# Performance work log

Hardware: AMD Instinct MI355X
Metric: run time of the kernel (lower is better)

Reference implementation:

```python
import jax, jax.numpy as jnp
import numpy as np

EMB, NH, NG, T_MAX = 2048, 16, 4, 2048
HD = EMB // NH          # 128
HPG = NH // NG          # 4
B, T = 2, 2048


def _rope_tables(t):
    inv_freq = 1.0 / (10000.0 ** (jnp.arange(0, HD, 2, dtype=jnp.float32) / HD))
    freqs = jnp.outer(jnp.arange(t, dtype=jnp.float32), inv_freq)  # [t, HD//2]
    return jnp.cos(freqs), jnp.sin(freqs)


def _apply_rope(x, cos, sin):
    # x: [..., t, HD], interleaved pairs (0::2 real, 1::2 imag)
    x1 = x[..., 0::2]
    x2 = x[..., 1::2]
    r1 = x1 * cos - x2 * sin
    r2 = x1 * sin + x2 * cos
    return jnp.stack([r1, r2], axis=-1).reshape(x.shape)


def setup_inputs() -> dict:
    key = jax.random.key(0)
    ks = jax.random.split(key, 5)
    s = 0.02
    return {
        "x": jax.random.normal(ks[0], (B, T, EMB), dtype=jnp.float32),
        "Wq": jax.random.normal(ks[1], (EMB, EMB), dtype=jnp.float32) * s,
        "Wk": jax.random.normal(ks[2], (NG * HD, EMB), dtype=jnp.float32) * s,
        "Wv": jax.random.normal(ks[3], (NG * HD, EMB), dtype=jnp.float32) * s,
        "Wo": jax.random.normal(ks[4], (EMB, EMB), dtype=jnp.float32) * s,
    }


def reference(x, Wq, Wk, Wv, Wo):
    b, t, _ = x.shape
    cos, sin = _rope_tables(t)  # [t, HD//2] each; broadcast over batch/heads

    # projections (torch Linear: x @ W.T)
    q = (x @ Wq.T).reshape(b, t, NH, HD).transpose(0, 2, 1, 3)  # [b, NH, t, HD]
    k = (x @ Wk.T).reshape(b, t, NG, HD).transpose(0, 2, 1, 3)  # [b, NG, t, HD]
    v = (x @ Wv.T).reshape(b, t, NG, HD).transpose(0, 2, 1, 3)  # [b, NG, t, HD]

    q = _apply_rope(q, cos, sin)
    k = _apply_rope(k, cos, sin)

    # grouped attention without materializing expanded K/V
    qg = q.reshape(b, NG, HPG, t, HD)                       # [b, g, h, t, d]
    scale = 1.0 / jnp.sqrt(jnp.asarray(HD, dtype=x.dtype))
    scores = jnp.einsum('bghtd,bgsd->bghts', qg, k) * scale  # [b, g, h, t, s]

    causal = jnp.tril(jnp.ones((t, t), dtype=bool))
    scores = jnp.where(causal, scores, jnp.finfo(scores.dtype).min)
    attn = jax.nn.softmax(scores, axis=-1)

    out = jnp.einsum('bghts,bgsd->bghtd', attn, v)           # [b, g, h, t, d]
    out = out.reshape(b, NH, t, HD).transpose(0, 2, 1, 3).reshape(b, t, EMB)
    return out @ Wo.T
```

## Files before the change

### kernel.cpp

```cpp
#include <hip/hip_runtime.h>
#include <stdint.h>
#include <math.h>

#define EMB 2048
#define NHq 16
#define NGk 4
#define HD 128
#define Bb 2
#define Tt 2048
#define MROWS (Bb*Tt)
#define QKVN 3072
#define NQT 32

typedef __bf16 bf16x8 __attribute__((ext_vector_type(8)));
typedef float f32x4 __attribute__((ext_vector_type(4)));
typedef unsigned int u32x4 __attribute__((ext_vector_type(4)));
typedef unsigned short u16;
typedef unsigned int u32;

__device__ __forceinline__ u16 f2bf(float f) {
    unsigned int u = __float_as_uint(f);
    u += 0x7fff + ((u >> 16) & 1);
    return (u16)(u >> 16);
}
__device__ __forceinline__ float bf2f(u16 u) {
    return __uint_as_float(((u32)u) << 16);
}
__device__ __forceinline__ u32 cvt_pk_bf16(float lo, float hi) {
    u32 r;
    asm("v_cvt_pk_bf16_f32 %0, %1, %2" : "=v"(r) : "v"(lo), "v"(hi));
    return r;
}

#define GLOAD_LDS16(g, l) \
    __builtin_amdgcn_global_load_lds((const __attribute__((address_space(1))) void*)(g), \
                                     (__attribute__((address_space(3))) void*)(l), 16, 0, 0)

__global__ void cast_bf16_kernel(const float* __restrict__ src, u16* __restrict__ dst, int n4) {
    int i = blockIdx.x * blockDim.x + threadIdx.x;
    if (i < n4) {
        float4 v = reinterpret_cast<const float4*>(src)[i];
        ushort4 o;
        o.x = f2bf(v.x); o.y = f2bf(v.y); o.z = f2bf(v.z); o.w = f2bf(v.w);
        reinterpret_cast<ushort4*>(dst)[i] = o;
    }
}

__global__ void wcast_kernel(const float* __restrict__ Wq, const float* __restrict__ Wk,
                             const float* __restrict__ Wv, const float* __restrict__ Wo,
                             u16* __restrict__ dst) {
    int i = blockIdx.x * blockDim.x + threadIdx.x;
    const float* src; int local;
    if (i < 1048576)      { src = Wq; local = i; }
    else if (i < 1310720) { src = Wk; local = i - 1048576; }
    else if (i < 1572864) { src = Wv; local = i - 1310720; }
    else                  { src = Wo; local = i - 1572864; }
    float4 v = reinterpret_cast<const float4*>(src)[local];
    ushort4 o;
    o.x = f2bf(v.x); o.y = f2bf(v.y); o.z = f2bf(v.z); o.w = f2bf(v.w);
    reinterpret_cast<ushort4*>(dst)[i] = o;
}

__global__ void rope_tables_kernel(float* __restrict__ ctab, float* __restrict__ stab) {
    int t = blockIdx.x, i = threadIdx.x;
    float inv = powf(10000.f, -2.f * (float)i / (float)HD);
    float ang = (float)t * inv;
    ctab[t * 64 + i] = cosf(ang);
    stab[t * 64 + i] = sinf(ang);
}

__global__ void rope_qk_kernel(const u16* __restrict__ lin, const float* __restrict__ ctab,
                               const float* __restrict__ stab, u16* __restrict__ Qb,
                               u16* __restrict__ Kb, float qscale) {
    int i = threadIdx.x;
    int tt = blockIdx.x * 4 + threadIdx.y;
    int hh = blockIdx.y, b = blockIdx.z;
    int coloff; u16* out; float scale;
    if (hh < NHq) { coloff = hh * HD; scale = qscale;
                    out = Qb + (((size_t)(b * NHq + hh)) * Tt + tt) * HD; }
    else { int g = hh - NHq; coloff = EMB + g * HD; scale = 1.f;
           out = Kb + (((size_t)(b * NGk + g)) * Tt + tt) * HD; }
    u32 pair = *reinterpret_cast<const u32*>(&lin[((size_t)(b * Tt + tt)) * QKVN + coloff + 2 * i]);
    float x1 = bf2f((u16)(pair & 0xffff)), x2 = bf2f((u16)(pair >> 16));
    float c = ctab[tt * 64 + i], s = stab[tt * 64 + i];
    ushort2 o;
    o.x = f2bf((x1 * c - x2 * s) * scale);
    o.y = f2bf((x1 * s + x2 * c) * scale);
    *reinterpret_cast<ushort2*>(&out[2 * i]) = o;
}

__global__ void vtrans_kernel(const u16* __restrict__ lin, u16* __restrict__ vt) {
    int tx = threadIdx.x, dy = threadIdx.y;
    int tt = blockIdx.x * 64 + tx;
    int g = blockIdx.y, b = blockIdx.z;
    int ttp = (tt & ~31) | (((tt >> 2) & 3) * 8 + ((tt >> 4) & 1) * 4 + (tt & 3));
    const u16* src = &lin[((size_t)(b * Tt + tt)) * QKVN + EMB + NGk * HD + g * HD];
    u16* dst = &vt[(((size_t)(b * NGk + g)) * HD) * Tt + ttp];
    #pragma unroll
    for (int k = 0; k < 16; ++k) {
        int d = dy + k * 8;
        dst[(size_t)d * Tt] = src[d];
    }
}

template<int OUTBF>
__global__ __launch_bounds__(256) void gemm_bt(const u16* __restrict__ A, const u16* __restrict__ W,
                                               void* __restrict__ Cout, int M, int N, int K) {
    __shared__ u16 Atile[128 * 32];
    __shared__ u16 Btile[128 * 32];
    const int brow = blockIdx.x * 128;
    const int bcol = blockIdx.y * 128;
    const int t = threadIdx.x;
    const int w = t >> 6, l = t & 63;
    const int lr = l & 15, lq = l >> 4;
    const int wr = (w >> 1) * 64, wc = (w & 1) * 64;
    f32x4 acc[4][4] = {};
    const int nkt = K >> 5;
    for (int kt = 0; kt < nkt; ++kt) {
        const int k0 = kt * 32;
        #pragma unroll
        for (int i = 0; i < 2; ++i) {
            int f = i * 256 + t;
            int row = f >> 2, cb = (f & 3) * 8;
            GLOAD_LDS16(A + (size_t)(brow + row) * K + k0 + cb, &Atile[(i * 256 + w * 64) * 8]);
            GLOAD_LDS16(W + (size_t)(bcol + row) * K + k0 + cb, &Btile[(i * 256 + w * 64) * 8]);
        }
        __syncthreads();
        bf16x8 a[4], b[4];
        #pragma unroll
        for (int m = 0; m < 4; ++m)
            a[m] = *reinterpret_cast<const bf16x8*>(&Atile[(wr + m * 16 + lr) * 32 + lq * 8]);
        #pragma unroll
        for (int n = 0; n < 4; ++n)
            b[n] = *reinterpret_cast<const bf16x8*>(&Btile[(wc + n * 16 + lr) * 32 + lq * 8]);
        #pragma unroll
        for (int m = 0; m < 4; ++m)
            #pragma unroll
            for (int n = 0; n < 4; ++n)
                acc[m][n] = __builtin_amdgcn_mfma_f32_16x16x32_bf16(a[m], b[n], acc[m][n], 0, 0, 0);
        __syncthreads();
    }
    #pragma unroll
    for (int m = 0; m < 4; ++m)
        #pragma unroll
        for (int n = 0; n < 4; ++n)
            #pragma unroll
            for (int r = 0; r < 4; ++r) {
                size_t idx = (size_t)(brow + wr + m * 16 + lq * 4 + r) * N + bcol + wc + n * 16 + lr;
                if (OUTBF) ((u16*)Cout)[idx] = f2bf(acc[m][n][r]);
                else       ((float*)Cout)[idx] = acc[m][n][r];
            }
}

__global__ __launch_bounds__(512) void flash_attn(const u16* __restrict__ Q, const u16* __restrict__ K,
                                                  const u16* __restrict__ Vt, u16* __restrict__ Out) {
    __shared__ __align__(16) char smem[69632];
    u16* KldsBase = (u16*)smem;
    u16* VldsBase = (u16*)(smem + 32768);
    const int h = blockIdx.y;
    const int b = blockIdx.z;
    const int ilo = (b == 0) ? blockIdx.x : (NQT / 2 - 1 - blockIdx.x);
    const int ihi = NQT - 1 - ilo;
    const int g = h >> 2;
    const int t = threadIdx.x;
    const int w = t >> 6, l = t & 63;
    const int wq = w & 3, half = w >> 2;
    const int lr = l & 15, lq = l >> 4;

    const size_t qhead = ((size_t)(b * NHq + h)) * Tt;
    const size_t qblo = (qhead + ilo * 64 + wq * 16) * HD;
    const size_t qbhi = (qhead + ihi * 64 + wq * 16) * HD;
    bf16x8 qfl[4], qfh[4];
    #pragma unroll
    for (int d = 0; d < 4; ++d) {
        qfl[d] = *reinterpret_cast<const bf16x8*>(&Q[qblo + (size_t)lr * HD + d * 32 + lq * 8]);
        qfh[d] = *reinterpret_cast<const bf16x8*>(&Q[qbhi + (size_t)lr * HD + d * 32 + lq * 8]);
    }
    bf16x8 ones;
    #pragma unroll
    for (int j = 0; j < 8; ++j) ones[j] = (__bf16)1.0f;

    f32x4 ol[8] = {}, oh[8] = {};
    f32x4 lsl = {}, lsh = {};

    const int qlo = ilo * 64 + wq * 16 + lr;
    const int qhi = ihi * 64 + wq * 16 + lr;
    const size_t kbase  = ((size_t)(b * NGk + g)) * Tt * HD;
    const size_t vtbase = ((size_t)(b * NGk + g)) * HD * Tt;
    const int nkt = NQT - ilo;

    int kofs[2], vofs[2];
    #pragma unroll
    for (int j = 0; j < 2; ++j) {
        int krow = j * 32 + w * 4 + (l >> 4);
        kofs[j] = krow * HD + (((l & 15) ^ (krow & 7)) * 8);
        int vrow = j * 64 + w * 8 + (l >> 3);
        vofs[j] = vrow * (int)Tt + (((l & 7) ^ (vrow & 7)) * 8);
    }

    #pragma unroll
    for (int j = 0; j < 2; ++j) {
        GLOAD_LDS16(K + kbase + kofs[j], KldsBase + (j * 512 + w * 64) * 8);
        GLOAD_LDS16(Vt + vtbase + vofs[j], VldsBase + (j * 512 + w * 64) * 8);
    }
    int cur = 0;

    for (int kt = 0; kt < nkt; ++kt) {
        const int kp0 = kt * 64;
        __syncthreads();
        if (kt + 1 < nkt) {
            #pragma unroll
            for (int j = 0; j < 2; ++j) {
                GLOAD_LDS16(K + kbase + (size_t)(kp0 + 64) * HD + kofs[j],
                            KldsBase + (cur ^ 1) * 8192 + (j * 512 + w * 64) * 8);
                GLOAD_LDS16(Vt + vtbase + (kp0 + 64) + vofs[j],
                            VldsBase + (cur ^ 1) * 8192 + (j * 512 + w * 64) * 8);
            }
        }
        const char* Kb = smem + cur * 16384;
        const char* Vb = smem + 32768 + cur * 16384;

        const bool lo_act = (kt <= ilo);
        f32x4 sl[2] = {}, sh[2] = {};
        __builtin_amdgcn_s_setprio(1);
        #pragma unroll
        for (int ct = 0; ct < 2; ++ct) {
            #pragma unroll
            for (int d = 0; d < 4; ++d) {
                int row = half * 32 + ct * 16 + lr;
                int bo = row * 256 + ((d * 64 + lq * 16) ^ ((row & 7) << 4));
                bf16x8 kf = *reinterpret_cast<const bf16x8*>(Kb + bo);
                sh[ct] = __builtin_amdgcn_mfma_f32_16x16x32_bf16(kf, qfh[d], sh[ct], 0, 0, 0);
                if (lo_act) sl[ct] = __builtin_amdgcn_mfma_f32_16x16x32_bf16(kf, qfl[d], sl[ct], 0, 0, 0);
            }
        }
        __builtin_amdgcn_s_setprio(0);

        const int kvb = kp0 + half * 32 + lq * 4;
        bf16x8 pfh, pfl;
        {
            const bool diag = (kt == nkt - 1);
            float e[2][4];
            #pragma unroll
            for (int ct = 0; ct < 2; ++ct)
                #pragma unroll
                for (int r = 0; r < 4; ++r)
                    e[ct][r] = exp2f(sh[ct][r]);
            if (diag) {
                #pragma unroll
                for (int ct = 0; ct < 2; ++ct)
                    #pragma unroll
                    for (int r = 0; r < 4; ++r)
                        if (kvb + ct * 16 + r > qhi) e[ct][r] = 0.f;
            }
            u32x4 pk;
            pk[0] = cvt_pk_bf16(e[0][0], e[0][1]);
            pk[1] = cvt_pk_bf16(e[0][2], e[0][3]);
            pk[2] = cvt_pk_bf16(e[1][0], e[1][1]);
            pk[3] = cvt_pk_bf16(e[1][2], e[1][3]);
            pfh = __builtin_bit_cast(bf16x8, pk);
        }
        if (lo_act) {
            const bool diag = (kt == ilo);
            float e[2][4];
            #pragma unroll
            for (int ct = 0; ct < 2; ++ct)
                #pragma unroll
                for (int r = 0; r < 4; ++r)
                    e[ct][r] = exp2f(sl[ct][r]);
            if (diag) {
                #pragma unroll
                for (int ct = 0; ct < 2; ++ct)
                    #pragma unroll
                    for (int r = 0; r < 4; ++r)
                        if (kvb + ct * 16 + r > qlo) e[ct][r] = 0.f;
            }
            u32x4 pk;
            pk[0] = cvt_pk_bf16(e[0][0], e[0][1]);
            pk[1] = cvt_pk_bf16(e[0][2], e[0][3]);
            pk[2] = cvt_pk_bf16(e[1][0], e[1][1]);
            pk[3] = cvt_pk_bf16(e[1][2], e[1][3]);
            pfl = __builtin_bit_cast(bf16x8, pk);
        }

        __builtin_amdgcn_s_setprio(1);
        #pragma unroll
        for (int n = 0; n < 8; ++n) {
            int vrow = n * 16 + lr;
            int bv = vrow * 128 + ((half * 64 + lq * 16) ^ ((vrow & 7) << 4));
            bf16x8 vf = *reinterpret_cast<const bf16x8*>(Vb + bv);
            oh[n] = __builtin_amdgcn_mfma_f32_16x16x32_bf16(vf, pfh, oh[n], 0, 0, 0);
            if (lo_act) ol[n] = __builtin_amdgcn_mfma_f32_16x16x32_bf16(vf, pfl, ol[n], 0, 0, 0);
        }
        lsh = __builtin_amdgcn_mfma_f32_16x16x32_bf16(ones, pfh, lsh, 0, 0, 0);
        if (lo_act) lsl = __builtin_amdgcn_mfma_f32_16x16x32_bf16(ones, pfl, lsl, 0, 0, 0);
        __builtin_amdgcn_s_setprio(0);
        cur ^= 1;
    }

    __syncthreads();
    float* Osh = (float*)smem;
    float* Lsh = (float*)(smem + 128 * 132 * 4);
    if (half == 1) {
        #pragma unroll
        for (int n = 0; n < 8; ++n) {
            *reinterpret_cast<f32x4*>(&Osh[(wq * 32 + lr) * 132 + n * 16 + lq * 4]) = oh[n];
            *reinterpret_cast<f32x4*>(&Osh[(wq * 32 + 16 + lr) * 132 + n * 16 + lq * 4]) = ol[n];
        }
        if (lq == 0) {
            Lsh[wq * 32 + lr] = lsh[0];
            Lsh[wq * 32 + 16 + lr] = lsl[0];
        }
    }
    __syncthreads();
    if (half == 0) {
        const float invh = 1.f / (lsh[0] + Lsh[wq * 32 + lr]);
        const float invl = 1.f / (lsl[0] + Lsh[wq * 32 + 16 + lr]);
        u16* outh = Out + ((size_t)(b * Tt) + ihi * 64 + wq * 16 + lr) * EMB + h * HD;
        u16* outl = Out + ((size_t)(b * Tt) + ilo * 64 + wq * 16 + lr) * EMB + h * HD;
        #pragma unroll
        for (int n = 0; n < 8; ++n) {
            f32x4 sh4 = *reinterpret_cast<const f32x4*>(&Osh[(wq * 32 + lr) * 132 + n * 16 + lq * 4]);
            f32x4 sl4 = *reinterpret_cast<const f32x4*>(&Osh[(wq * 32 + 16 + lr) * 132 + n * 16 + lq * 4]);
            uint2 ph, pl;
            ph.x = cvt_pk_bf16((oh[n][0] + sh4[0]) * invh, (oh[n][1] + sh4[1]) * invh);
            ph.y = cvt_pk_bf16((oh[n][2] + sh4[2]) * invh, (oh[n][3] + sh4[3]) * invh);
            pl.x = cvt_pk_bf16((ol[n][0] + sl4[0]) * invl, (ol[n][1] + sl4[1]) * invl);
            pl.y = cvt_pk_bf16((ol[n][2] + sl4[2]) * invl, (ol[n][3] + sl4[3]) * invl);
            *reinterpret_cast<uint2*>(&outh[n * 16 + lq * 4]) = ph;
            *reinterpret_cast<uint2*>(&outl[n * 16 + lq * 4]) = pl;
        }
    }
}

extern "C" void kernel_launch(void* const* d_in, const int* in_sizes, int n_in,
                              void* d_out, int out_size, void* d_ws, size_t ws_size,
                              hipStream_t stream) {
    (void)in_sizes; (void)n_in; (void)out_size; (void)ws_size;
    const float* x  = (const float*)d_in[0];
    const float* Wq = (const float*)d_in[1];
    const float* Wk = (const float*)d_in[2];
    const float* Wv = (const float*)d_in[3];
    const float* Wo = (const float*)d_in[4];
    float* out = (float*)d_out;

    char* ws = (char*)d_ws;
    size_t off = 0;
    auto alloc = [&](size_t bytes) { char* p = ws + off; off += (bytes + 255) & ~(size_t)255; return p; };

    u16* w_bf    = (u16*)alloc((size_t)(QKVN * EMB + EMB * EMB) * 2);
    u16* x_bf    = (u16*)alloc((size_t)MROWS * EMB * 2);
    u16* qkv_lin = (u16*)alloc((size_t)MROWS * QKVN * 4);
    u16* Qb      = (u16*)alloc((size_t)Bb * NHq * Tt * HD * 2);
    u16* Kb      = (u16*)alloc((size_t)Bb * NGk * Tt * HD * 2);
    u16* Vtb     = (u16*)alloc((size_t)Bb * NGk * HD * Tt * 2);
    float* ctab  = (float*)alloc((size_t)Tt * 64 * 4);
    float* stab  = (float*)alloc((size_t)Tt * 64 * 4);
    u16* attnout = qkv_lin;

    u16* wo_bf = w_bf + (size_t)QKVN * EMB;

    cast_bf16_kernel<<<(MROWS * EMB / 4 + 255) / 256, 256, 0, stream>>>(x, x_bf, MROWS * EMB / 4);
    wcast_kernel<<<(QKVN * EMB + EMB * EMB) / 4 / 256, 256, 0, stream>>>(Wq, Wk, Wv, Wo, w_bf);
    rope_tables_kernel<<<Tt, 64, 0, stream>>>(ctab, stab);

    gemm_bt<1><<<dim3(MROWS / 128, QKVN / 128), 256, 0, stream>>>(x_bf, w_bf, qkv_lin, MROWS, QKVN, EMB);

    const float qscale = 1.44269504088896f / sqrtf((float)HD);
    rope_qk_kernel<<<dim3(Tt / 4, NHq + NGk, Bb), dim3(64, 4), 0, stream>>>(qkv_lin, ctab, stab, Qb, Kb, qscale);
    vtrans_kernel<<<dim3(Tt / 64, NGk, Bb), dim3(64, 8), 0, stream>>>(qkv_lin, Vtb);

    flash_attn<<<dim3(NQT / 2, NHq, Bb), 512, 0, stream>>>(Qb, Kb, Vtb, attnout);

    gemm_bt<0><<<dim3(MROWS / 128, EMB / 128), 256, 0, stream>>>(attnout, wo_bf, out, MROWS, EMB, EMB);
}
```

Measured before the change: 240.7 us.

## Software-pipeline attention loop: overlap QK/softmax of tile p with PV of tile p-1

Restructures the flash attention main loop so each iteration computes scores and softmax for the current KV tile while doing the PV accumulation for the previous tile. The V buffer becomes triple-buffered to allow this, which raises LDS use to 80KB, and the loop gains one extra epilogue iteration. The aim is to let exp and convert work interleave with MFMA work so fewer matrix-core cycles sit idle. The cost is higher register pressure from carrying the previous probability fragments, plus larger LDS that may reduce occupancy.

```diff
diff --git a/kernel.cpp b/kernel.cpp
--- a/kernel.cpp
+++ b/kernel.cpp
@@ -154,7 +154,7 @@
 
 __global__ __launch_bounds__(512) void flash_attn(const u16* __restrict__ Q, const u16* __restrict__ K,
                                                   const u16* __restrict__ Vt, u16* __restrict__ Out) {
-    __shared__ __align__(16) char smem[69632];
+    __shared__ __align__(16) char smem[81920];
     u16* KldsBase = (u16*)smem;
     u16* VldsBase = (u16*)(smem + 32768);
     const int h = blockIdx.y;
@@ -203,99 +203,107 @@
         GLOAD_LDS16(K + kbase + kofs[j], KldsBase + (j * 512 + w * 64) * 8);
         GLOAD_LDS16(Vt + vtbase + vofs[j], VldsBase + (j * 512 + w * 64) * 8);
     }
-    int cur = 0;
-
-    for (int kt = 0; kt < nkt; ++kt) {
-        const int kp0 = kt * 64;
-        __syncthreads();
-        if (kt + 1 < nkt) {
+    __syncthreads();
+
+    bf16x8 pfh_c, pfl_c;
+
+    for (int p = 0; p <= nkt; ++p) {
+        if (p + 1 < nkt) {
+            const size_t kp1 = (size_t)(p + 1) * 64;
+            u16* kd = KldsBase + ((p + 1) & 1) * 8192;
+            u16* vd = VldsBase + ((p + 1) % 3) * 8192;
             #pragma unroll
             for (int j = 0; j < 2; ++j) {
-                GLOAD_LDS16(K + kbase + (size_t)(kp0 + 64) * HD + kofs[j],
-                            KldsBase + (cur ^ 1) * 8192 + (j * 512 + w * 64) * 8);
-                GLOAD_LDS16(Vt + vtbase + (kp0 + 64) + vofs[j],
-                            VldsBase + (cur ^ 1) * 8192 + (j * 512 + w * 64) * 8);
-            }
-        }
-        const char* Kb = smem + cur * 16384;
-        const char* Vb = smem + 32768 + cur * 16384;
-
-        const bool lo_act = (kt <= ilo);
-        f32x4 sl[2] = {}, sh[2] = {};
-        __builtin_amdgcn_s_setprio(1);
-        #pragma unroll
-        for (int ct = 0; ct < 2; ++ct) {
-            #pragma unroll
-            for (int d = 0; d < 4; ++d) {
-                int row = half * 32 + ct * 16 + lr;
-                int bo = row * 256 + ((d * 64 + lq * 16) ^ ((row & 7) << 4));
-                bf16x8 kf = *reinterpret_cast<const bf16x8*>(Kb + bo);
-                sh[ct] = __builtin_amdgcn_mfma_f32_16x16x32_bf16(kf, qfh[d], sh[ct], 0, 0, 0);
-                if (lo_act) sl[ct] = __builtin_amdgcn_mfma_f32_16x16x32_bf16(kf, qfl[d], sl[ct], 0, 0, 0);
-            }
-        }
-        __builtin_amdgcn_s_setprio(0);
-
-        const int kvb = kp0 + half * 32 + lq * 4;
-        bf16x8 pfh, pfl;
-        {
-            const bool diag = (kt == nkt - 1);
-            float e[2][4];
-            #pragma unroll
-            for (int ct = 0; ct < 2; ++ct)
+                GLOAD_LDS16(K + kbase + kp1 * HD + kofs[j], kd + (j * 512 + w * 64) * 8);
+                GLOAD_LDS16(Vt + vtbase + kp1 + vofs[j], vd + (j * 512 + w * 64) * 8);
+            }
+        }
+
+        const bool lo_p = (p <= ilo);
+        bf16x8 pfh_n, pfl_n;
+        if (p < nkt) {
+            const char* Kb = smem + (p & 1) * 16384;
+            f32x4 sl[2] = {}, sh[2] = {};
+            __builtin_amdgcn_s_setprio(1);
+            #pragma unroll
+            for (int ct = 0; ct < 2; ++ct) {
                 #pragma unroll
-                for (int r = 0; r < 4; ++r)
-                    e[ct][r] = exp2f(sh[ct][r]);
-            if (diag) {
+                for (int d = 0; d < 4; ++d) {
+                    int row = half * 32 + ct * 16 + lr;
+                    int bo = row * 256 + ((d * 64 + lq * 16) ^ ((row & 7) << 4));
+                    bf16x8 kf = *reinterpret_cast<const bf16x8*>(Kb + bo);
+                    sh[ct] = __builtin_amdgcn_mfma_f32_16x16x32_bf16(kf, qfh[d], sh[ct], 0, 0, 0);
+                    if (lo_p) sl[ct] = __builtin_amdgcn_mfma_f32_16x16x32_bf16(kf, qfl[d], sl[ct], 0, 0, 0);
+                }
+            }
+            __builtin_amdgcn_s_setprio(0);
+
+            const int kvb = p * 64 + half * 32 + lq * 4;
+            {
+                const bool diag = (p == nkt - 1);
+                float e[2][4];
                 #pragma unroll
                 for (int ct = 0; ct < 2; ++ct)
                     #pragma unroll
                     for (int r = 0; r < 4; ++r)
-                        if (kvb + ct * 16 + r > qhi) e[ct][r] = 0.f;
-            }
-            u32x4 pk;
-            pk[0] = cvt_pk_bf16(e[0][0], e[0][1]);
-            pk[1] = cvt_pk_bf16(e[0][2], e[0][3]);
-            pk[2] = cvt_pk_bf16(e[1][0], e[1][1]);
-            pk[3] = cvt_pk_bf16(e[1][2], e[1][3]);
-            pfh = __builtin_bit_cast(bf16x8, pk);
-        }
-        if (lo_act) {
-            const bool diag = (kt == ilo);
-            float e[2][4];
-            #pragma unroll
-            for (int ct = 0; ct < 2; ++ct)
-                #pragma unroll
-                for (int r = 0; r < 4; ++r)
-                    e[ct][r] = exp2f(sl[ct][r]);
-            if (diag) {
+                        e[ct][r] = exp2f(sh[ct][r]);
+                if (diag) {
+                    #pragma unroll
+                    for (int ct = 0; ct < 2; ++ct)
+                        #pragma unroll
+                        for (int r = 0; r < 4; ++r)
+                            if (kvb + ct * 16 + r > qhi) e[ct][r] = 0.f;
+                }
+                u32x4 pk;
+                pk[0] = cvt_pk_bf16(e[0][0], e[0][1]);
+                pk[1] = cvt_pk_bf16(e[0][2], e[0][3]);
+                pk[2] = cvt_pk_bf16(e[1][0], e[1][1]);
+                pk[3] = cvt_pk_bf16(e[1][2], e[1][3]);
+                pfh_n = __builtin_bit_cast(bf16x8, pk);
+            }
+            if (lo_p) {
+                const bool diag = (p == ilo);
+                float e[2][4];
                 #pragma unroll
                 for (int ct = 0; ct < 2; ++ct)
                     #pragma unroll
                     for (int r = 0; r < 4; ++r)
-                        if (kvb + ct * 16 + r > qlo) e[ct][r] = 0.f;
-            }
-            u32x4 pk;
-            pk[0] = cvt_pk_bf16(e[0][0], e[0][1]);
-            pk[1] = cvt_pk_bf16(e[0][2], e[0][3]);
-            pk[2] = cvt_pk_bf16(e[1][0], e[1][1]);
-            pk[3] = cvt_pk_bf16(e[1][2], e[1][3]);
-            pfl = __builtin_bit_cast(bf16x8, pk);
-        }
-
-        __builtin_amdgcn_s_setprio(1);
-        #pragma unroll
-        for (int n = 0; n < 8; ++n) {
-            int vrow = n * 16 + lr;
-            int bv = vrow * 128 + ((half * 64 + lq * 16) ^ ((vrow & 7) << 4));
-            bf16x8 vf = *reinterpret_cast<const bf16x8*>(Vb + bv);
-            oh[n] = __builtin_amdgcn_mfma_f32_16x16x32_bf16(vf, pfh, oh[n], 0, 0, 0);
-            if (lo_act) ol[n] = __builtin_amdgcn_mfma_f32_16x16x32_bf16(vf, pfl, ol[n], 0, 0, 0);
-        }
-        lsh = __builtin_amdgcn_mfma_f32_16x16x32_bf16(ones, pfh, lsh, 0, 0, 0);
-        if (lo_act) lsl = __builtin_amdgcn_mfma_f32_16x16x32_bf16(ones, pfl, lsl, 0, 0, 0);
-        __builtin_amdgcn_s_setprio(0);
-        cur ^= 1;
+                        e[ct][r] = exp2f(sl[ct][r]);
+                if (diag) {
+                    #pragma unroll
+                    for (int ct = 0; ct < 2; ++ct)
+                        #pragma unroll
+                        for (int r = 0; r < 4; ++r)
+                            if (kvb + ct * 16 + r > qlo) e[ct][r] = 0.f;
+                }
+                u32x4 pk;
+                pk[0] = cvt_pk_bf16(e[0][0], e[0][1]);
+                pk[1] = cvt_pk_bf16(e[0][2], e[0][3]);
+                pk[2] = cvt_pk_bf16(e[1][0], e[1][1]);
+                pk[3] = cvt_pk_bf16(e[1][2], e[1][3]);
+                pfl_n = __builtin_bit_cast(bf16x8, pk);
+            }
+        }
+
+        if (p >= 1) {
+            const char* Vb = smem + 32768 + ((p - 1) % 3) * 16384;
+            const bool lo_prev = (p - 1 <= ilo);
+            __builtin_amdgcn_s_setprio(1);
+            #pragma unroll
+            for (int n = 0; n < 8; ++n) {
+                int vrow = n * 16 + lr;
+                int bv = vrow * 128 + ((half * 64 + lq * 16) ^ ((vrow & 7) << 4));
+                bf16x8 vf = *reinterpret_cast<const bf16x8*>(Vb + bv);
+                oh[n] = __builtin_amdgcn_mfma_f32_16x16x32_bf16(vf, pfh_c, oh[n], 0, 0, 0);
+                if (lo_prev) ol[n] = __builtin_amdgcn_mfma_f32_16x16x32_bf16(vf, pfl_c, ol[n], 0, 0, 0);
+            }
+            lsh = __builtin_amdgcn_mfma_f32_16x16x32_bf16(ones, pfh_c, lsh, 0, 0, 0);
+            if (lo_prev) lsl = __builtin_amdgcn_mfma_f32_16x16x32_bf16(ones, pfl_c, lsl, 0, 0, 0);
+            __builtin_amdgcn_s_setprio(0);
+        }
+        pfh_c = pfh_n;
+        pfl_c = pfl_n;
+        if (p + 1 < nkt) __syncthreads();
     }
 
     __syncthreads();
```

After: 246.4 us. +2.4%, slower.

## Load K/V fragments directly from global into registers, drop LDS staging

Applied to the files above, without the earlier changes.

Attention now reads K and V^T fragments straight from global memory into registers each tile, instead of double-buffering them through LDS with async global-to-LDS loads and barriers. The block index mapping is reordered so the heads sharing a KV group land in neighbouring blocks, which should improve L2 reuse of K/V. The epilogue reduction is split into two passes so LDS shrinks to about 34KB, allowing higher occupancy. The trade-off is that global-load latency is no longer hidden by prefetching, and each wave issues redundant global reads that it depends on via cache hits.

```diff
diff --git a/kernel.cpp b/kernel.cpp
--- a/kernel.cpp
+++ b/kernel.cpp
@@ -154,14 +154,13 @@
 
 __global__ __launch_bounds__(512) void flash_attn(const u16* __restrict__ Q, const u16* __restrict__ K,
                                                   const u16* __restrict__ Vt, u16* __restrict__ Out) {
-    __shared__ __align__(16) char smem[69632];
-    u16* KldsBase = (u16*)smem;
-    u16* VldsBase = (u16*)(smem + 32768);
-    const int h = blockIdx.y;
-    const int b = blockIdx.z;
-    const int ilo = (b == 0) ? blockIdx.x : (NQT / 2 - 1 - blockIdx.x);
+    __shared__ __align__(16) char smem[34816];
+    const int bx = blockIdx.x, by = blockIdx.y, bz = blockIdx.z;
+    const int g = bx & 3, b = (bx >> 2) & 1;
+    const int hh = (bx >> 3) | (bz << 1);
+    const int h = g * 4 + hh;
+    const int ilo = (hh & 1) ? (15 - by) : by;
     const int ihi = NQT - 1 - ilo;
-    const int g = h >> 2;
     const int t = threadIdx.x;
     const int w = t >> 6, l = t & 63;
     const int wq = w & 3, half = w >> 2;
@@ -185,53 +184,34 @@
 
     const int qlo = ilo * 64 + wq * 16 + lr;
     const int qhi = ihi * 64 + wq * 16 + lr;
-    const size_t kbase  = ((size_t)(b * NGk + g)) * Tt * HD;
-    const size_t vtbase = ((size_t)(b * NGk + g)) * HD * Tt;
+    const u16* Kp = K + ((size_t)(b * NGk + g)) * Tt * HD + (size_t)(half * 32 + lr) * HD + lq * 8;
+    const u16* Vp = Vt + ((size_t)(b * NGk + g)) * HD * Tt + (size_t)lr * Tt + half * 32 + lq * 8;
     const int nkt = NQT - ilo;
-
-    int kofs[2], vofs[2];
-    #pragma unroll
-    for (int j = 0; j < 2; ++j) {
-        int krow = j * 32 + w * 4 + (l >> 4);
-        kofs[j] = krow * HD + (((l & 15) ^ (krow & 7)) * 8);
-        int vrow = j * 64 + w * 8 + (l >> 3);
-        vofs[j] = vrow * (int)Tt + (((l & 7) ^ (vrow & 7)) * 8);
-    }
-
-    #pragma unroll
-    for (int j = 0; j < 2; ++j) {
-        GLOAD_LDS16(K + kbase + kofs[j], KldsBase + (j * 512 + w * 64) * 8);
-        GLOAD_LDS16(Vt + vtbase + vofs[j], VldsBase + (j * 512 + w * 64) * 8);
-    }
-    int cur = 0;
 
     for (int kt = 0; kt < nkt; ++kt) {
         const int kp0 = kt * 64;
-        __syncthreads();
-        if (kt + 1 < nkt) {
-            #pragma unroll
-            for (int j = 0; j < 2; ++j) {
-                GLOAD_LDS16(K + kbase + (size_t)(kp0 + 64) * HD + kofs[j],
-                            KldsBase + (cur ^ 1) * 8192 + (j * 512 + w * 64) * 8);
-                GLOAD_LDS16(Vt + vtbase + (kp0 + 64) + vofs[j],
-                            VldsBase + (cur ^ 1) * 8192 + (j * 512 + w * 64) * 8);
-            }
-        }
-        const char* Kb = smem + cur * 16384;
-        const char* Vb = smem + 32768 + cur * 16384;
-
-        const bool lo_act = (kt <= ilo);
+        const bool lo_p = (kt <= ilo);
+        const u16* Kt = Kp + (size_t)kp0 * HD;
+        uint4 kr[2][4];
+        #pragma unroll
+        for (int ct = 0; ct < 2; ++ct)
+            #pragma unroll
+            for (int d = 0; d < 4; ++d)
+                kr[ct][d] = *reinterpret_cast<const uint4*>(Kt + (size_t)(ct * 16) * HD + d * 32);
+        uint4 vr[8];
+        #pragma unroll
+        for (int n = 0; n < 8; ++n)
+            vr[n] = *reinterpret_cast<const uint4*>(Vp + (size_t)(n * 16) * Tt + kp0);
+
         f32x4 sl[2] = {}, sh[2] = {};
         __builtin_amdgcn_s_setprio(1);
         #pragma unroll
         for (int ct = 0; ct < 2; ++ct) {
             #pragma unroll
             for (int d = 0; d < 4; ++d) {
-                int row = half * 32 + ct * 16 + lr;
-                int bo = row * 256 + ((d * 64 + lq * 16) ^ ((row & 7) << 4));
-                bf16x8 kf = *reinterpret_cast<const bf16x8*>(Kb + bo);
+                bf16x8 kf = __builtin_bit_cast(bf16x8, kr[ct][d]);
                 sh[ct] = __builtin_amdgcn_mfma_f32_16x16x32_bf16(kf, qfh[d], sh[ct], 0, 0, 0);
-                if (lo_act) sl[ct] = __builtin_amdgcn_mfma_f32_16x16x32_bf16(kf, qfl[d], sl[ct], 0, 0, 0);
+                if (lo_p) sl[ct] = __builtin_amdgcn_mfma_f32_16x16x32_bf16(kf, qfl[d], sl[ct], 0, 0, 0);
             }
         }
         __builtin_amdgcn_s_setprio(0);
@@ -260,7 +240,7 @@
             pk[3] = cvt_pk_bf16(e[1][2], e[1][3]);
             pfh = __builtin_bit_cast(bf16x8, pk);
         }
-        if (lo_act) {
+        if (lo_p) {
             const bool diag = (kt == ilo);
             float e[2][4];
             #pragma unroll
@@ -286,49 +266,56 @@
         __builtin_amdgcn_s_setprio(1);
         #pragma unroll
         for (int n = 0; n < 8; ++n) {
-            int vrow = n * 16 + lr;
-            int bv = vrow * 128 + ((half * 64 + lq * 16) ^ ((vrow & 7) << 4));
-            bf16x8 vf = *reinterpret_cast<const bf16x8*>(Vb + bv);
+            bf16x8 vf = __builtin_bit_cast(bf16x8, vr[n]);
             oh[n] = __builtin_amdgcn_mfma_f32_16x16x32_bf16(vf, pfh, oh[n], 0, 0, 0);
-            if (lo_act) ol[n] = __builtin_amdgcn_mfma_f32_16x16x32_bf16(vf, pfl, ol[n], 0, 0, 0);
+            if (lo_p) ol[n] = __builtin_amdgcn_mfma_f32_16x16x32_bf16(vf, pfl, ol[n], 0, 0, 0);
         }
         lsh = __builtin_amdgcn_mfma_f32_16x16x32_bf16(ones, pfh, lsh, 0, 0, 0);
-        if (lo_act) lsl = __builtin_amdgcn_mfma_f32_16x16x32_bf16(ones, pfl, lsl, 0, 0, 0);
+        if (lo_p) lsl = __builtin_amdgcn_mfma_f32_16x16x32_bf16(ones, pfl, lsl, 0, 0, 0);
         __builtin_amdgcn_s_setprio(0);
-        cur ^= 1;
-    }
-
+    }
+
+    float* Osh = (float*)smem;
+    float* Lsh = (float*)(smem + 64 * 132 * 4);
+    const int row = wq * 16 + lr;
     __syncthreads();
-    float* Osh = (float*)smem;
-    float* Lsh = (float*)(smem + 128 * 132 * 4);
     if (half == 1) {
         #pragma unroll
-        for (int n = 0; n < 8; ++n) {
-            *reinterpret_cast<f32x4*>(&Osh[(wq * 32 + lr) * 132 + n * 16 + lq * 4]) = oh[n];
-            *reinterpret_cast<f32x4*>(&Osh[(wq * 32 + 16 + lr) * 132 + n * 16 + lq * 4]) = ol[n];
-        }
-        if (lq == 0) {
-            Lsh[wq * 32 + lr] = lsh[0];
-            Lsh[wq * 32 + 16 + lr] = lsl[0];
-        }
+        for (int n = 0; n < 8; ++n)
+            *reinterpret_cast<f32x4*>(&Osh[row * 132 + n * 16 + lq * 4]) = oh[n];
+        if (lq == 0) Lsh[row] = lsh[0];
     }
     __syncthreads();
     if (half == 0) {
-        const float invh = 1.f / (lsh[0] + Lsh[wq * 32 + lr]);
-        const float invl = 1.f / (lsl[0] + Lsh[wq * 32 + 16 + lr]);
-        u16* outh = Out + ((size_t)(b * Tt) + ihi * 64 + wq * 16 + lr) * EMB + h * HD;
-        u16* outl = Out + ((size_t)(b * Tt) + ilo * 64 + wq * 16 + lr) * EMB + h * HD;
+        const float inv = 1.f / (lsh[0] + Lsh[row]);
+        u16* outp = Out + ((size_t)(b * Tt) + ihi * 64 + row) * EMB + h * HD;
         #pragma unroll
         for (int n = 0; n < 8; ++n) {
-            f32x4 sh4 = *reinterpret_cast<const f32x4*>(&Osh[(wq * 32 + lr) * 132 + n * 16 + lq * 4]);
-            f32x4 sl4 = *reinterpret_cast<const f32x4*>(&Osh[(wq * 32 + 16 + lr) * 132 + n * 16 + lq * 4]);
-            uint2 ph, pl;
-            ph.x = cvt_pk_bf16((oh[n][0] + sh4[0]) * invh, (oh[n][1] + sh4[1]) * invh);
-            ph.y = cvt_pk_bf16((oh[n][2] + sh4[2]) * invh, (oh[n][3] + sh4[3]) * invh);
-            pl.x = cvt_pk_bf16((ol[n][0] + sl4[0]) * invl, (ol[n][1] + sl4[1]) * invl);
-            pl.y = cvt_pk_bf16((ol[n][2] + sl4[2]) * invl, (ol[n][3] + sl4[3]) * invl);
-            *reinterpret_cast<uint2*>(&outh[n * 16 + lq * 4]) = ph;
-            *reinterpret_cast<uint2*>(&outl[n * 16 + lq * 4]) = pl;
+            f32x4 s4 = *reinterpret_cast<const f32x4*>(&Osh[row * 132 + n * 16 + lq * 4]);
+            uint2 p;
+            p.x = cvt_pk_bf16((oh[n][0] + s4[0]) * inv, (oh[n][1] + s4[1]) * inv);
+            p.y = cvt_pk_bf16((oh[n][2] + s4[2]) * inv, (oh[n][3] + s4[3]) * inv);
+            *reinterpret_cast<uint2*>(&outp[n * 16 + lq * 4]) = p;
+        }
+    }
+    __syncthreads();
+    if (half == 1) {
+        #pragma unroll
+        for (int n = 0; n < 8; ++n)
+            *reinterpret_cast<f32x4*>(&Osh[row * 132 + n * 16 + lq * 4]) = ol[n];
+        if (lq == 0) Lsh[row] = lsl[0];
+    }
+    __syncthreads();
+    if (half == 0) {
+        const float inv = 1.f / (lsl[0] + Lsh[row]);
+        u16* outp = Out + ((size_t)(b * Tt) + ilo * 64 + row) * EMB + h * HD;
+        #pragma unroll
+        for (int n = 0; n < 8; ++n) {
+            f32x4 s4 = *reinterpret_cast<const f32x4*>(&Osh[row * 132 + n * 16 + lq * 4]);
+            uint2 p;
+            p.x = cvt_pk_bf16((ol[n][0] + s4[0]) * inv, (ol[n][1] + s4[1]) * inv);
+            p.y = cvt_pk_bf16((ol[n][2] + s4[2]) * inv, (ol[n][3] + s4[3]) * inv);
+            *reinterpret_cast<uint2*>(&outp[n * 16 + lq * 4]) = p;
         }
     }
 }
@@ -370,7 +357,7 @@
     rope_qk_kernel<<<dim3(Tt / 4, NHq + NGk, Bb), dim3(64, 4), 0, stream>>>(qkv_lin, ctab, stab, Qb, Kb, qscale);
     vtrans_kernel<<<dim3(Tt / 64, NGk, Bb), dim3(64, 8), 0, stream>>>(qkv_lin, Vtb);
 
-    flash_attn<<<dim3(NQT / 2, NHq, Bb), 512, 0, stream>>>(Qb, Kb, Vtb, attnout);
+    flash_attn<<<dim3(16, 16, 2), 512, 0, stream>>>(Qb, Kb, Vtb, attnout);
 
     gemm_bt<0><<<dim3(MROWS / 128, EMB / 128), 256, 0, stream>>>(attnout, wo_bf, out, MROWS, EMB, EMB);
 }
```

Result: slower. 395.5 us (+64.3%).

## Restructure flash attention to contiguous 128-row query tiles with 4 waves

Applied to the files above, without the earlier changes.

Replaces the paired low/high query-tile scheme (512 threads, two halves splitting the KV tile and reducing through LDS) with 256-thread blocks that each own a contiguous 128-row query tile. Each wave handles 32 query rows over the full 64-key tile, so the cross-half LDS reduction at the end goes away. Load balance now comes from reversing the tile order for the second batch instead of pairing a short tile with a long one. The risk is causal load imbalance, since block work ranges from 2 to 32 KV tiles, and waves whose rows are already fully masked sit idle while still joining the per-tile barriers.

```diff
diff --git a/kernel.cpp b/kernel.cpp
--- a/kernel.cpp
+++ b/kernel.cpp
@@ -152,183 +152,170 @@
             }
 }
 
-__global__ __launch_bounds__(512) void flash_attn(const u16* __restrict__ Q, const u16* __restrict__ K,
+__global__ __launch_bounds__(256) void flash_attn(const u16* __restrict__ Q, const u16* __restrict__ K,
                                                   const u16* __restrict__ Vt, u16* __restrict__ Out) {
-    __shared__ __align__(16) char smem[69632];
-    u16* KldsBase = (u16*)smem;
-    u16* VldsBase = (u16*)(smem + 32768);
+    __shared__ __align__(16) char smem[65536];
     const int h = blockIdx.y;
     const int b = blockIdx.z;
-    const int ilo = (b == 0) ? blockIdx.x : (NQT / 2 - 1 - blockIdx.x);
-    const int ihi = NQT - 1 - ilo;
+    const int qt = (b == 0) ? blockIdx.x : (15 - blockIdx.x);
     const int g = h >> 2;
     const int t = threadIdx.x;
     const int w = t >> 6, l = t & 63;
-    const int wq = w & 3, half = w >> 2;
     const int lr = l & 15, lq = l >> 4;
+    const int qbase = qt * 128 + w * 32;
 
     const size_t qhead = ((size_t)(b * NHq + h)) * Tt;
-    const size_t qblo = (qhead + ilo * 64 + wq * 16) * HD;
-    const size_t qbhi = (qhead + ihi * 64 + wq * 16) * HD;
-    bf16x8 qfl[4], qfh[4];
+    bf16x8 qf0[4], qf1[4];
     #pragma unroll
     for (int d = 0; d < 4; ++d) {
-        qfl[d] = *reinterpret_cast<const bf16x8*>(&Q[qblo + (size_t)lr * HD + d * 32 + lq * 8]);
-        qfh[d] = *reinterpret_cast<const bf16x8*>(&Q[qbhi + (size_t)lr * HD + d * 32 + lq * 8]);
+        qf0[d] = *reinterpret_cast<const bf16x8*>(&Q[(qhead + qbase + lr) * HD + d * 32 + lq * 8]);
+        qf1[d] = *reinterpret_cast<const bf16x8*>(&Q[(qhead + qbase + 16 + lr) * HD + d * 32 + lq * 8]);
     }
     bf16x8 ones;
     #pragma unroll
     for (int j = 0; j < 8; ++j) ones[j] = (__bf16)1.0f;
 
-    f32x4 ol[8] = {}, oh[8] = {};
-    f32x4 lsl = {}, lsh = {};
-
-    const int qlo = ilo * 64 + wq * 16 + lr;
-    const int qhi = ihi * 64 + wq * 16 + lr;
+    f32x4 o0[8] = {}, o1[8] = {};
+    f32x4 ls0 = {}, ls1 = {};
+
+    const int q0 = qbase + lr;
+    const int q1 = qbase + 16 + lr;
+    const int lastvis = (qbase + 31) >> 6;
     const size_t kbase  = ((size_t)(b * NGk + g)) * Tt * HD;
     const size_t vtbase = ((size_t)(b * NGk + g)) * HD * Tt;
-    const int nkt = NQT - ilo;
-
-    int kofs[2], vofs[2];
-    #pragma unroll
-    for (int j = 0; j < 2; ++j) {
-        int krow = j * 32 + w * 4 + (l >> 4);
-        kofs[j] = krow * HD + (((l & 15) ^ (krow & 7)) * 8);
-        int vrow = j * 64 + w * 8 + (l >> 3);
-        vofs[j] = vrow * (int)Tt + (((l & 7) ^ (vrow & 7)) * 8);
-    }
-
-    #pragma unroll
-    for (int j = 0; j < 2; ++j) {
-        GLOAD_LDS16(K + kbase + kofs[j], KldsBase + (j * 512 + w * 64) * 8);
-        GLOAD_LDS16(Vt + vtbase + vofs[j], VldsBase + (j * 512 + w * 64) * 8);
-    }
-    int cur = 0;
+    const int nkt = 2 * (qt + 1);
+
+    int kofs[4], vofs[4];
+    #pragma unroll
+    for (int j = 0; j < 4; ++j) {
+        int krow = j * 16 + (t >> 4);
+        kofs[j] = krow * HD + (((t & 15) ^ (krow & 7)) * 8);
+        int vrow = j * 32 + (t >> 3);
+        vofs[j] = vrow * (int)Tt + (((t & 7) ^ (vrow & 7)) * 8);
+    }
+
+    #pragma unroll
+    for (int j = 0; j < 4; ++j) {
+        GLOAD_LDS16(K + kbase + kofs[j], smem + (j * 256 + t) * 16);
+        GLOAD_LDS16(Vt + vtbase + vofs[j], smem + 32768 + (j * 256 + t) * 16);
+    }
 
     for (int kt = 0; kt < nkt; ++kt) {
-        const int kp0 = kt * 64;
         __syncthreads();
         if (kt + 1 < nkt) {
-            #pragma unroll
-            for (int j = 0; j < 2; ++j) {
-                GLOAD_LDS16(K + kbase + (size_t)(kp0 + 64) * HD + kofs[j],
-                            KldsBase + (cur ^ 1) * 8192 + (j * 512 + w * 64) * 8);
-                GLOAD_LDS16(Vt + vtbase + (kp0 + 64) + vofs[j],
-                            VldsBase + (cur ^ 1) * 8192 + (j * 512 + w * 64) * 8);
-            }
-        }
-        const char* Kb = smem + cur * 16384;
-        const char* Vb = smem + 32768 + cur * 16384;
-
-        const bool lo_act = (kt <= ilo);
-        f32x4 sl[2] = {}, sh[2] = {};
+            const size_t kp1 = (size_t)(kt + 1) * 64;
+            char* kd = smem + ((kt + 1) & 1) * 16384;
+            char* vd = smem + 32768 + ((kt + 1) & 1) * 16384;
+            #pragma unroll
+            for (int j = 0; j < 4; ++j) {
+                GLOAD_LDS16(K + kbase + kp1 * HD + kofs[j], kd + (j * 256 + t) * 16);
+                GLOAD_LDS16(Vt + vtbase + kp1 + vofs[j], vd + (j * 256 + t) * 16);
+            }
+        }
+        if (kt > lastvis) continue;
+        const char* Kb = smem + (kt & 1) * 16384;
+        const char* Vb = smem + 32768 + (kt & 1) * 16384;
+
+        f32x4 s0[4] = {}, s1[4] = {};
         __builtin_amdgcn_s_setprio(1);
         #pragma unroll
-        for (int ct = 0; ct < 2; ++ct) {
+        for (int ct = 0; ct < 4; ++ct) {
             #pragma unroll
             for (int d = 0; d < 4; ++d) {
-                int row = half * 32 + ct * 16 + lr;
+                int row = ct * 16 + lr;
                 int bo = row * 256 + ((d * 64 + lq * 16) ^ ((row & 7) << 4));
                 bf16x8 kf = *reinterpret_cast<const bf16x8*>(Kb + bo);
-                sh[ct] = __builtin_amdgcn_mfma_f32_16x16x32_bf16(kf, qfh[d], sh[ct], 0, 0, 0);
-                if (lo_act) sl[ct] = __builtin_amdgcn_mfma_f32_16x16x32_bf16(kf, qfl[d], sl[ct], 0, 0, 0);
+                s0[ct] = __builtin_amdgcn_mfma_f32_16x16x32_bf16(kf, qf0[d], s0[ct], 0, 0, 0);
+                s1[ct] = __builtin_amdgcn_mfma_f32_16x16x32_bf16(kf, qf1[d], s1[ct], 0, 0, 0);
             }
         }
         __builtin_amdgcn_s_setprio(0);
 
-        const int kvb = kp0 + half * 32 + lq * 4;
-        bf16x8 pfh, pfl;
+        const bool diag = (kt == lastvis);
+        const int kvb = kt * 64 + lq * 4;
+        bf16x8 pf0[2], pf1[2];
         {
-            const bool diag = (kt == nkt - 1);
-            float e[2][4];
-            #pragma unroll
-            for (int ct = 0; ct < 2; ++ct)
+            float e[4][4];
+            #pragma unroll
+            for (int ct = 0; ct < 4; ++ct)
                 #pragma unroll
                 for (int r = 0; r < 4; ++r)
-                    e[ct][r] = exp2f(sh[ct][r]);
+                    e[ct][r] = exp2f(s0[ct][r]);
             if (diag) {
                 #pragma unroll
-                for (int ct = 0; ct < 2; ++ct)
+                for (int ct = 0; ct < 4; ++ct)
                     #pragma unroll
                     for (int r = 0; r < 4; ++r)
-                        if (kvb + ct * 16 + r > qhi) e[ct][r] = 0.f;
-            }
-            u32x4 pk;
-            pk[0] = cvt_pk_bf16(e[0][0], e[0][1]);
-            pk[1] = cvt_pk_bf16(e[0][2], e[0][3]);
-            pk[2] = cvt_pk_bf16(e[1][0], e[1][1]);
-            pk[3] = cvt_pk_bf16(e[1][2], e[1][3]);
-            pfh = __builtin_bit_cast(bf16x8, pk);
-        }
-        if (lo_act) {
-            const bool diag = (kt == ilo);
-            float e[2][4];
-            #pragma unroll
-            for (int ct = 0; ct < 2; ++ct)
+                        if (kvb + ct * 16 + r > q0) e[ct][r] = 0.f;
+            }
+            #pragma unroll
+            for (int ks = 0; ks < 2; ++ks) {
+                u32x4 pk;
+                pk[0] = cvt_pk_bf16(e[ks * 2][0], e[ks * 2][1]);
+                pk[1] = cvt_pk_bf16(e[ks * 2][2], e[ks * 2][3]);
+                pk[2] = cvt_pk_bf16(e[ks * 2 + 1][0], e[ks * 2 + 1][1]);
+                pk[3] = cvt_pk_bf16(e[ks * 2 + 1][2], e[ks * 2 + 1][3]);
+                pf0[ks] = __builtin_bit_cast(bf16x8, pk);
+            }
+        }
+        {
+            float e[4][4];
+            #pragma unroll
+            for (int ct = 0; ct < 4; ++ct)
                 #pragma unroll
                 for (int r = 0; r < 4; ++r)
-                    e[ct][r] = exp2f(sl[ct][r]);
+                    e[ct][r] = exp2f(s1[ct][r]);
             if (diag) {
                 #pragma unroll
-                for (int ct = 0; ct < 2; ++ct)
+                for (int ct = 0; ct < 4; ++ct)
                     #pragma unroll
                     for (int r = 0; r < 4; ++r)
-                        if (kvb + ct * 16 + r > qlo) e[ct][r] = 0.f;
-            }
-            u32x4 pk;
-            pk[0] = cvt_pk_bf16(e[0][0], e[0][1]);
-            pk[1] = cvt_pk_bf16(e[0][2], e[0][3]);
-            pk[2] = cvt_pk_bf16(e[1][0], e[1][1]);
-            pk[3] = cvt_pk_bf16(e[1][2], e[1][3]);
-            pfl = __builtin_bit_cast(bf16x8, pk);
+                        if (kvb + ct * 16 + r > q1) e[ct][r] = 0.f;
+            }
+            #pragma unroll
+            for (int ks = 0; ks < 2; ++ks) {
+                u32x4 pk;
+                pk[0] = cvt_pk_bf16(e[ks * 2][0], e[ks * 2][1]);
+                pk[1] = cvt_pk_bf16(e[ks * 2][2], e[ks * 2][3]);
+                pk[2] = cvt_pk_bf16(e[ks * 2 + 1][0], e[ks * 2 + 1][1]);
+                pk[3] = cvt_pk_bf16(e[ks * 2 + 1][2], e[ks * 2 + 1][3]);
+                pf1[ks] = __builtin_bit_cast(bf16x8, pk);
+            }
         }
 
         __builtin_amdgcn_s_setprio(1);
         #pragma unroll
         for (int n = 0; n < 8; ++n) {
             int vrow = n * 16 + lr;
-            int bv = vrow * 128 + ((half * 64 + lq * 16) ^ ((vrow & 7) << 4));
-            bf16x8 vf = *reinterpret_cast<const bf16x8*>(Vb + bv);
-            oh[n] = __builtin_amdgcn_mfma_f32_16x16x32_bf16(vf, pfh, oh[n], 0, 0, 0);
-            if (lo_act) ol[n] = __builtin_amdgcn_mfma_f32_16x16x32_bf16(vf, pfl, ol[n], 0, 0, 0);
-        }
-        lsh = __builtin_amdgcn_mfma_f32_16x16x32_bf16(ones, pfh, lsh, 0, 0, 0);
-        if (lo_act) lsl = __builtin_amdgcn_mfma_f32_16x16x32_bf16(ones, pfl, lsl, 0, 0, 0);
+            #pragma unroll
+            for (int ks = 0; ks < 2; ++ks) {
+                int bv = vrow * 128 + ((ks * 64 + lq * 16) ^ ((vrow & 7) << 4));
+                bf16x8 vf = *reinterpret_cast<const bf16x8*>(Vb + bv);
+                o0[n] = __builtin_amdgcn_mfma_f32_16x16x32_bf16(vf, pf0[ks], o0[n], 0, 0, 0);
+                o1[n] = __builtin_amdgcn_mfma_f32_16x16x32_bf16(vf, pf1[ks], o1[n], 0, 0, 0);
+            }
+        }
+        ls0 = __builtin_amdgcn_mfma_f32_16x16x32_bf16(ones, pf0[0], ls0, 0, 0, 0);
+        ls0 = __builtin_amdgcn_mfma_f32_16x16x32_bf16(ones, pf0[1], ls0, 0, 0, 0);
+        ls1 = __builtin_amdgcn_mfma_f32_16x16x32_bf16(ones, pf1[0], ls1, 0, 0, 0);
+        ls1 = __builtin_amdgcn_mfma_f32_16x16x32_bf16(ones, pf1[1], ls1, 0, 0, 0);
         __builtin_amdgcn_s_setprio(0);
-        cur ^= 1;
-    }
-
-    __syncthreads();
-    float* Osh = (float*)smem;
-    float* Lsh = (float*)(smem + 128 * 132 * 4);
-    if (half == 1) {
+    }
+
+    {
+        const float inv0 = 1.f / ls0[0];
+        const float inv1 = 1.f / ls1[0];
+        u16* out0 = Out + ((size_t)(b * Tt) + q0) * EMB + h * HD;
+        u16* out1 = Out + ((size_t)(b * Tt) + q1) * EMB + h * HD;
         #pragma unroll
         for (int n = 0; n < 8; ++n) {
-            *reinterpret_cast<f32x4*>(&Osh[(wq * 32 + lr) * 132 + n * 16 + lq * 4]) = oh[n];
-            *reinterpret_cast<f32x4*>(&Osh[(wq * 32 + 16 + lr) * 132 + n * 16 + lq * 4]) = ol[n];
-        }
-        if (lq == 0) {
-            Lsh[wq * 32 + lr] = lsh[0];
-            Lsh[wq * 32 + 16 + lr] = lsl[0];
-        }
-    }
-    __syncthreads();
-    if (half == 0) {
-        const float invh = 1.f / (lsh[0] + Lsh[wq * 32 + lr]);
-        const float invl = 1.f / (lsl[0] + Lsh[wq * 32 + 16 + lr]);
-        u16* outh = Out + ((size_t)(b * Tt) + ihi * 64 + wq * 16 + lr) * EMB + h * HD;
-        u16* outl = Out + ((size_t)(b * Tt) + ilo * 64 + wq * 16 + lr) * EMB + h * HD;
-        #pragma unroll
-        for (int n = 0; n < 8; ++n) {
-            f32x4 sh4 = *reinterpret_cast<const f32x4*>(&Osh[(wq * 32 + lr) * 132 + n * 16 + lq * 4]);
-            f32x4 sl4 = *reinterpret_cast<const f32x4*>(&Osh[(wq * 32 + 16 + lr) * 132 + n * 16 + lq * 4]);
-            uint2 ph, pl;
-            ph.x = cvt_pk_bf16((oh[n][0] + sh4[0]) * invh, (oh[n][1] + sh4[1]) * invh);
-            ph.y = cvt_pk_bf16((oh[n][2] + sh4[2]) * invh, (oh[n][3] + sh4[3]) * invh);
-            pl.x = cvt_pk_bf16((ol[n][0] + sl4[0]) * invl, (ol[n][1] + sl4[1]) * invl);
-            pl.y = cvt_pk_bf16((ol[n][2] + sl4[2]) * invl, (ol[n][3] + sl4[3]) * invl);
-            *reinterpret_cast<uint2*>(&outh[n * 16 + lq * 4]) = ph;
-            *reinterpret_cast<uint2*>(&outl[n * 16 + lq * 4]) = pl;
+            uint2 p0, p1;
+            p0.x = cvt_pk_bf16(o0[n][0] * inv0, o0[n][1] * inv0);
+            p0.y = cvt_pk_bf16(o0[n][2] * inv0, o0[n][3] * inv0);
+            p1.x = cvt_pk_bf16(o1[n][0] * inv1, o1[n][1] * inv1);
+            p1.y = cvt_pk_bf16(o1[n][2] * inv1, o1[n][3] * inv1);
+            *reinterpret_cast<uint2*>(&out0[n * 16 + lq * 4]) = p0;
+            *reinterpret_cast<uint2*>(&out1[n * 16 + lq * 4]) = p1;
         }
     }
 }
@@ -370,7 +357,7 @@
     rope_qk_kernel<<<dim3(Tt / 4, NHq + NGk, Bb), dim3(64, 4), 0, stream>>>(qkv_lin, ctab, stab, Qb, Kb, qscale);
     vtrans_kernel<<<dim3(Tt / 64, NGk, Bb), dim3(64, 8), 0, stream>>>(qkv_lin, Vtb);
 
-    flash_attn<<<dim3(NQT / 2, NHq, Bb), 512, 0, stream>>>(Qb, Kb, Vtb, attnout);
+    flash_attn<<<dim3(16, NHq, Bb), 256, 0, stream>>>(Qb, Kb, Vtb, attnout);
 
     gemm_bt<0><<<dim3(MROWS / 128, EMB / 128), 256, 0, stream>>>(attnout, wo_bf, out, MROWS, EMB, EMB);
 }
```

New measurement: 233.2 us. 3.1% less time.
